# Optimization experiments

Hardware: AMD Instinct MI355X
Metric: run time of the kernel (lower is better)

## Reference

```python
import jax, jax.numpy as jnp
import numpy as np

NUM_EMBEDDINGS = 1024
EMBEDDING_DIM = 64
COMMITMENT_COST = 0.25


def setup_inputs() -> dict:
    key = jax.random.key(0)
    k_in, k_w = jax.random.split(key)
    inputs = jax.random.normal(k_in, (32, 64, 32, 32), dtype=jnp.float32)
    # nn.Embedding weight initialized uniform(-1/K, 1/K)
    bound = 1.0 / NUM_EMBEDDINGS
    weight = jax.random.uniform(k_w, (NUM_EMBEDDINGS, EMBEDDING_DIM),
                                dtype=jnp.float32, minval=-bound, maxval=bound)
    return {"inputs": inputs, "weight": weight}


def reference(inputs, weight):
    # Flatten to [N, D] rows in embedding space
    flat = inputs.reshape(-1, EMBEDDING_DIM)  # [N, D]
    distances = (jnp.sum(flat * flat, axis=1, keepdims=True)
                 + jnp.sum(weight * weight, axis=1)
                 - 2.0 * jnp.matmul(flat, weight.T))
    encoding_indices = jnp.argmin(distances, axis=1)  # [N]
    quantized = weight[encoding_indices].reshape(inputs.shape)
    e_latent_loss = jnp.mean((jax.lax.stop_gradient(quantized) - inputs) ** 2)
    q_latent_loss = jnp.mean((quantized - jax.lax.stop_gradient(inputs)) ** 2)
    commitment_loss = COMMITMENT_COST * (q_latent_loss + e_latent_loss)
    # Straight-through estimator
    quantized = inputs + jax.lax.stop_gradient(quantized - inputs)
    return quantized, encoding_indices[:, None], commitment_loss
```

## Files before the change

### kernel.cpp

```cpp
#include <hip/hip_runtime.h>

#define NROWS  32768
#define DIM    64
#define KCODES 1024
#define NELEM  (NROWS * DIM)
#define CHUNKS 8
#define CPC    128
#define NBLK_B 512
#define RPB_B  64

typedef float v2f __attribute__((ext_vector_type(2)));

__device__ __forceinline__ float np_sumsq_f4(const float4* __restrict__ p) {
#pragma clang fp contract(off)
  float4 a = p[0], b = p[1];
  float r0 = a.x * a.x, r1 = a.y * a.y, r2 = a.z * a.z, r3 = a.w * a.w;
  float r4 = b.x * b.x, r5 = b.y * b.y, r6 = b.z * b.z, r7 = b.w * b.w;
#pragma unroll
  for (int i = 1; i < 8; ++i) {
    a = p[2 * i]; b = p[2 * i + 1];
    r0 += a.x * a.x; r1 += a.y * a.y; r2 += a.z * a.z; r3 += a.w * a.w;
    r4 += b.x * b.x; r5 += b.y * b.y; r6 += b.z * b.z; r7 += b.w * b.w;
  }
  return ((r0 + r1) + (r2 + r3)) + ((r4 + r5) + (r6 + r7));
}

__global__ __launch_bounds__(256, 4) void vq_dist(const float* __restrict__ x,
                                                  const float* __restrict__ w,
                                                  unsigned long long* __restrict__ keys,
                                                  double* __restrict__ loss,
                                                  unsigned int* __restrict__ cnt) {
  __shared__ float se[CPC];
  const int t = threadIdx.x;
  const int g = blockIdx.x >> 3;
  const int chunk = blockIdx.x & 7;
  const int c0 = chunk * CPC;

  if (blockIdx.x == 0 && t == 0) { *loss = 0.0; *cnt = 0u; }

  if (t < CPC)
    se[t] = np_sumsq_f4((const float4*)(w + (size_t)(c0 + t) * DIM));

  const int row = g * 256 + t;
  const float4* xr = (const float4*)(x + (size_t)row * DIM);
  const float sx = np_sumsq_f4(xr);

  v2f xv[32];
#pragma unroll
  for (int i = 0; i < 16; ++i) {
    float4 q = xr[i];
    xv[2 * i + 0] = (v2f){q.x, q.y};
    xv[2 * i + 1] = (v2f){q.z, q.w};
  }
#pragma unroll
  for (int i = 0; i < 32; ++i) asm volatile("" : "+v"(xv[i]));

  __syncthreads();

  const float4* wbase = (const float4*)w;
  float best_d = 3.4e38f;
  int best_c = c0;

#pragma unroll 2
  for (int j = 0; j < CPC; ++j) {
    const int c = c0 + j;
    const float4* wr = wbase + ((size_t)c << 4);
    v2f a0 = (v2f){0.f, 0.f}, a1 = (v2f){0.f, 0.f};
    v2f a2 = (v2f){0.f, 0.f}, a3 = (v2f){0.f, 0.f};
#pragma unroll
    for (int i = 0; i < 16; i += 2) {
      float4 q0 = wr[i];
      float4 q1 = wr[i + 1];
      a0 += (v2f){q0.x, q0.y} * xv[2 * i + 0];
      a1 += (v2f){q0.z, q0.w} * xv[2 * i + 1];
      a2 += (v2f){q1.x, q1.y} * xv[2 * i + 2];
      a3 += (v2f){q1.z, q1.w} * xv[2 * i + 3];
    }
    v2f s = (a0 + a1) + (a2 + a3);
    float dot = s.x + s.y;
    float ad = sx + se[j];
    float d = fmaf(-2.0f, dot, ad);
    if (d < best_d) { best_d = d; best_c = c; }
  }

  keys[((size_t)row << 3) | chunk] =
      ((unsigned long long)__float_as_uint(best_d) << 32) | (unsigned int)best_c;
}

__global__ __launch_bounds__(256) void vq_out(const float* __restrict__ x,
                                              const float* __restrict__ w,
                                              const unsigned long long* __restrict__ keys,
                                              float* __restrict__ outq,
                                              float* __restrict__ outidx,
                                              double* __restrict__ loss,
                                              unsigned int* __restrict__ cnt,
                                              float* __restrict__ outloss) {
  __shared__ int sidx[RPB_B];
  __shared__ double part[4];
  const int b = blockIdx.x, t = threadIdx.x;

  if (t < RPB_B) {
    const int row = b * RPB_B + t;
    const unsigned long long* kr = keys + ((size_t)row << 3);
    unsigned long long m = kr[0];
#pragma unroll
    for (int i = 1; i < 8; ++i) { unsigned long long k = kr[i]; if (k < m) m = k; }
    const int idx = (int)(unsigned int)(m & 0xFFFFFFFFull);
    outidx[row] = (float)idx;
    sidx[t] = idx;
  }
  __syncthreads();

  double acc = 0.0;
  const float4* x4 = (const float4*)x;
  float4* o4 = (float4*)outq;
#pragma unroll
  for (int i = 0; i < 4; ++i) {
    const int e = i * 256 + t;
    const int rl = e >> 4;
    const int d4 = e & 15;
    const size_t gofs = ((size_t)b * RPB_B + rl) * 16 + d4;
    float4 xvv = x4[gofs];
    const float4* wr = (const float4*)(w + (size_t)sidx[rl] * DIM);
    float4 wv = wr[d4];
    float tx = wv.x - xvv.x, ty = wv.y - xvv.y;
    float tz = wv.z - xvv.z, tw = wv.w - xvv.w;
    float4 q;
    q.x = xvv.x + tx; q.y = xvv.y + ty;
    q.z = xvv.z + tz; q.w = xvv.w + tw;
    o4[gofs] = q;
    acc += (double)tx * tx + (double)ty * ty + (double)tz * tz + (double)tw * tw;
  }

#pragma unroll
  for (int s = 32; s > 0; s >>= 1) acc += __shfl_down(acc, s, 64);
  if ((t & 63) == 0) part[t >> 6] = acc;
  __syncthreads();
  if (t == 0) {
    atomicAdd(loss, (part[0] + part[1]) + (part[2] + part[3]));
    __threadfence();
    unsigned int old = atomicAdd(cnt, 1u);
    if (old == NBLK_B - 1) {
      double L = atomicAdd(loss, 0.0);
      *outloss = 0.5f * (float)(L / (double)NELEM);
    }
  }
}

extern "C" void kernel_launch(void* const* d_in, const int* in_sizes, int n_in,
                              void* d_out, int out_size, void* d_ws, size_t ws_size,
                              hipStream_t stream) {
  const float* x = (const float*)d_in[0];
  const float* w = (const float*)d_in[1];

  float* outq    = (float*)d_out;
  float* outidx  = outq + NELEM;
  float* outloss = outidx + NROWS;

  char* wsb = (char*)d_ws;
  double* loss = (double*)wsb;
  unsigned int* cnt = (unsigned int*)(wsb + 64);
  unsigned long long* keys = (unsigned long long*)(wsb + 256);

  hipLaunchKernelGGL(vq_dist, dim3(1024),  dim3(256), 0, stream,
                     x, w, keys, loss, cnt);
  hipLaunchKernelGGL(vq_out,  dim3(NBLK_B), dim3(256), 0, stream,
                     x, w, keys, outq, outidx, loss, cnt, outloss);
}
```

Baseline: 152.9 us.

## Tile distance computation through swizzled LDS with register-blocked outer products

Replaces the per-thread row-vs-codebook dot loop, which streams codebook rows from global memory, with a 128-row by 128-code tile. Both operands are staged in XOR-swizzled shared memory, and each thread accumulates an 8x8 register block of packed FMAs. Row and code norms move to a separate prep kernel, and per-block argmin keys are reduced through LDS. The aim is to cut redundant global and cache loads and raise arithmetic intensity, at the cost of an extra launch, 64KB of LDS per block and lower occupancy.

```diff
diff --git a/kernel.cpp b/kernel.cpp
--- a/kernel.cpp
+++ b/kernel.cpp
@@ -4,8 +4,6 @@
 #define DIM    64
 #define KCODES 1024
 #define NELEM  (NROWS * DIM)
-#define CHUNKS 8
-#define CPC    128
 #define NBLK_B 512
 #define RPB_B  64
 
@@ -25,66 +23,122 @@
   return ((r0 + r1) + (r2 + r3)) + ((r4 + r5) + (r6 + r7));
 }
 
-__global__ __launch_bounds__(256, 4) void vq_dist(const float* __restrict__ x,
+__global__ __launch_bounds__(256) void vq_prep(const float* __restrict__ x,
+                                               const float* __restrict__ w,
+                                               float* __restrict__ sxv,
+                                               float* __restrict__ se,
+                                               double* __restrict__ loss,
+                                               unsigned int* __restrict__ cnt) {
+  const int t = blockIdx.x * 256 + threadIdx.x;
+  if (t == 0) { *loss = 0.0; *cnt = 0u; }
+  sxv[t] = np_sumsq_f4((const float4*)(x + (size_t)t * DIM));
+  if (t < KCODES) se[t] = np_sumsq_f4((const float4*)(w + (size_t)t * DIM));
+}
+
+__global__ __launch_bounds__(256, 2) void vq_dist(const float* __restrict__ x,
                                                   const float* __restrict__ w,
-                                                  unsigned long long* __restrict__ keys,
-                                                  double* __restrict__ loss,
-                                                  unsigned int* __restrict__ cnt) {
-  __shared__ float se[CPC];
+                                                  const float* __restrict__ sxv,
+                                                  const float* __restrict__ seg,
+                                                  unsigned long long* __restrict__ keys) {
+  __shared__ float xs[128 * 64];
+  __shared__ float ws[64 * 128];
   const int t = threadIdx.x;
-  const int g = blockIdx.x >> 3;
-  const int chunk = blockIdx.x & 7;
-  const int c0 = chunk * CPC;
-
-  if (blockIdx.x == 0 && t == 0) { *loss = 0.0; *cnt = 0u; }
-
-  if (t < CPC)
-    se[t] = np_sumsq_f4((const float4*)(w + (size_t)(c0 + t) * DIM));
-
-  const int row = g * 256 + t;
-  const float4* xr = (const float4*)(x + (size_t)row * DIM);
-  const float sx = np_sumsq_f4(xr);
-
-  v2f xv[32];
-#pragma unroll
-  for (int i = 0; i < 16; ++i) {
-    float4 q = xr[i];
-    xv[2 * i + 0] = (v2f){q.x, q.y};
-    xv[2 * i + 1] = (v2f){q.z, q.w};
-  }
-#pragma unroll
-  for (int i = 0; i < 32; ++i) asm volatile("" : "+v"(xv[i]));
-
-  __syncthreads();
-
-  const float4* wbase = (const float4*)w;
-  float best_d = 3.4e38f;
-  int best_c = c0;
+  const int rg = blockIdx.x >> 3;
+  const int cc = blockIdx.x & 7;
+  const int row0 = rg * 128;
+  const int c0 = cc * 128;
+
+  {
+    const float4* xg = (const float4*)x + (size_t)row0 * 16;
+    const float4* wg = (const float4*)w + (size_t)c0 * 16;
+    float4* xs4 = (float4*)xs;
+#pragma unroll
+    for (int i = 0; i < 8; ++i) {
+      const int g = t + 256 * i;
+      const int rr = g >> 4, f4 = g & 15;
+      xs4[rr * 16 + (f4 ^ (rr & 15))] = xg[g];
+      float4 u = wg[g];
+      const int k0 = f4 * 4;
+      const int clo = rr & 3, chi = rr >> 2;
+      ws[(k0 + 0) * 128 + ((chi ^ ((k0 + 0) & 31)) << 2) + clo] = u.x;
+      ws[(k0 + 1) * 128 + ((chi ^ ((k0 + 1) & 31)) << 2) + clo] = u.y;
+      ws[(k0 + 2) * 128 + ((chi ^ ((k0 + 2) & 31)) << 2) + clo] = u.z;
+      ws[(k0 + 3) * 128 + ((chi ^ ((k0 + 3) & 31)) << 2) + clo] = u.w;
+    }
+  }
+  __syncthreads();
+
+  const int m = t & 15, a = t >> 4;
+  v2f acc[8][4];
+#pragma unroll
+  for (int j = 0; j < 8; ++j)
+#pragma unroll
+    for (int p = 0; p < 4; ++p) acc[j][p] = (v2f){0.f, 0.f};
+
+  const float4* xs4 = (const float4*)xs;
+  const float4* ws4 = (const float4*)ws;
 
 #pragma unroll 2
-  for (int j = 0; j < CPC; ++j) {
-    const int c = c0 + j;
-    const float4* wr = wbase + ((size_t)c << 4);
-    v2f a0 = (v2f){0.f, 0.f}, a1 = (v2f){0.f, 0.f};
-    v2f a2 = (v2f){0.f, 0.f}, a3 = (v2f){0.f, 0.f};
-#pragma unroll
-    for (int i = 0; i < 16; i += 2) {
-      float4 q0 = wr[i];
-      float4 q1 = wr[i + 1];
-      a0 += (v2f){q0.x, q0.y} * xv[2 * i + 0];
-      a1 += (v2f){q0.z, q0.w} * xv[2 * i + 1];
-      a2 += (v2f){q1.x, q1.y} * xv[2 * i + 2];
-      a3 += (v2f){q1.z, q1.w} * xv[2 * i + 3];
-    }
-    v2f s = (a0 + a1) + (a2 + a3);
-    float dot = s.x + s.y;
-    float ad = sx + se[j];
-    float d = fmaf(-2.0f, dot, ad);
-    if (d < best_d) { best_d = d; best_c = c; }
-  }
-
-  keys[((size_t)row << 3) | chunk] =
-      ((unsigned long long)__float_as_uint(best_d) << 32) | (unsigned int)best_c;
+  for (int kb = 0; kb < 16; ++kb) {
+    float4 xf[8];
+#pragma unroll
+    for (int j = 0; j < 8; ++j)
+      xf[j] = xs4[(m + 16 * j) * 16 + (kb ^ m)];
+    v2f wf[4][4];
+#pragma unroll
+    for (int kk = 0; kk < 4; ++kk) {
+      const int k = kb * 4 + kk, sw = k & 31;
+      float4 u0 = ws4[k * 32 + (a ^ sw)];
+      float4 u1 = ws4[k * 32 + ((a + 16) ^ sw)];
+      wf[kk][0] = (v2f){u0.x, u0.y}; wf[kk][1] = (v2f){u0.z, u0.w};
+      wf[kk][2] = (v2f){u1.x, u1.y}; wf[kk][3] = (v2f){u1.z, u1.w};
+    }
+#pragma unroll
+    for (int j = 0; j < 8; ++j) {
+#pragma unroll
+      for (int p = 0; p < 4; ++p) {
+        acc[j][p] += (v2f){xf[j].x, xf[j].x} * wf[0][p];
+        acc[j][p] += (v2f){xf[j].y, xf[j].y} * wf[1][p];
+        acc[j][p] += (v2f){xf[j].z, xf[j].z} * wf[2][p];
+        acc[j][p] += (v2f){xf[j].w, xf[j].w} * wf[3][p];
+      }
+    }
+  }
+
+  unsigned long long bk[8];
+#pragma unroll
+  for (int j = 0; j < 8; ++j) {
+    const float sx = sxv[row0 + m + 16 * j];
+    unsigned long long best = ~0ull;
+#pragma unroll
+    for (int p = 0; p < 4; ++p) {
+      const int cb = c0 + 4 * a + ((p < 2) ? 2 * p : 64 + 2 * (p - 2));
+      const float d0 = fmaf(-2.0f, acc[j][p].x, sx + seg[cb]);
+      const float d1 = fmaf(-2.0f, acc[j][p].y, sx + seg[cb + 1]);
+      const unsigned long long k0v =
+          ((unsigned long long)__float_as_uint(d0) << 32) | (unsigned int)cb;
+      const unsigned long long k1v =
+          ((unsigned long long)__float_as_uint(d1) << 32) | (unsigned int)(cb + 1);
+      if (k0v < best) best = k0v;
+      if (k1v < best) best = k1v;
+    }
+    bk[j] = best;
+  }
+
+  __syncthreads();
+  unsigned long long* kred = (unsigned long long*)xs;
+#pragma unroll
+  for (int j = 0; j < 8; ++j) kred[(m + 16 * j) * 17 + a] = bk[j];
+  __syncthreads();
+  if (t < 128) {
+    unsigned long long mn = kred[t * 17];
+#pragma unroll
+    for (int q = 1; q < 16; ++q) {
+      const unsigned long long kq = kred[t * 17 + q];
+      if (kq < mn) mn = kq;
+    }
+    keys[((size_t)(row0 + t) << 3) | cc] = mn;
+  }
 }
 
 __global__ __launch_bounds__(256) void vq_out(const float* __restrict__ x,
@@ -102,10 +156,10 @@
   if (t < RPB_B) {
     const int row = b * RPB_B + t;
     const unsigned long long* kr = keys + ((size_t)row << 3);
-    unsigned long long m = kr[0];
-#pragma unroll
-    for (int i = 1; i < 8; ++i) { unsigned long long k = kr[i]; if (k < m) m = k; }
-    const int idx = (int)(unsigned int)(m & 0xFFFFFFFFull);
+    unsigned long long mn = kr[0];
+#pragma unroll
+    for (int i = 1; i < 8; ++i) { unsigned long long k = kr[i]; if (k < mn) mn = k; }
+    const int idx = (int)(unsigned int)(mn & 0xFFFFFFFFull);
     outidx[row] = (float)idx;
     sidx[t] = idx;
   }
@@ -160,10 +214,14 @@
   char* wsb = (char*)d_ws;
   double* loss = (double*)wsb;
   unsigned int* cnt = (unsigned int*)(wsb + 64);
-  unsigned long long* keys = (unsigned long long*)(wsb + 256);
-
-  hipLaunchKernelGGL(vq_dist, dim3(1024),  dim3(256), 0, stream,
-                     x, w, keys, loss, cnt);
+  float* sxv = (float*)(wsb + 4096);
+  float* se  = (float*)(wsb + 4096 + 131072);
+  unsigned long long* keys = (unsigned long long*)(wsb + 139264);
+
+  hipLaunchKernelGGL(vq_prep, dim3(128),  dim3(256), 0, stream,
+                     x, w, sxv, se, loss, cnt);
+  hipLaunchKernelGGL(vq_dist, dim3(2048), dim3(256), 0, stream,
+                     x, w, sxv, se, keys);
   hipLaunchKernelGGL(vq_out,  dim3(NBLK_B), dim3(256), 0, stream,
                      x, w, keys, outq, outidx, loss, cnt, outloss);
 }
```

New measurement: 143.6 us. 1.06x faster.
